# Performance work log

Hardware: AMD Instinct MI355X
Metric: run time of the kernel (lower is better)

The kernel has to match this reference:

```python
import jax, jax.numpy as jnp
import numpy as np

S, D = 8192, 2048      # sequence length, feature dim (input_size)
H, E, K, L = 64, 64, 2, 64  # gate hidden, expert count, top-k, expert layer_size
EPS = 1e-12            # torch F.normalize eps


def setup_inputs() -> dict:
    key = jax.random.key(0)
    ks = jax.random.split(key, 5)
    x = jax.random.normal(ks[0], (S, D), dtype=jnp.float32)
    # torch nn.Linear weights have shape [out_features, in_features]
    Wg_in = jax.random.normal(ks[1], (H, D), dtype=jnp.float32) * 0.02   # gate.input
    Wg_lin = jax.random.normal(ks[2], (E, H), dtype=jnp.float32) * 0.02  # gate.linear
    Wg_out = jax.random.normal(ks[3], (1, S), dtype=jnp.float32) * 0.02  # gate.output
    We = jax.random.normal(ks[4], (E, L, D), dtype=jnp.float32) * 0.02   # expert weight bank
    return {"x": x, "Wg_in": Wg_in, "Wg_lin": Wg_lin, "Wg_out": Wg_out, "We": We}


def reference(x, Wg_in, Wg_lin, Wg_out, We):
    # --- SparseGate (eval mode: dropout = identity) ---
    h = x @ Wg_in.T                         # [S, H]
    logits = h @ Wg_lin.T                   # [S, E]
    scores = (logits.T @ Wg_out.T)[:, 0]    # Linear(S,1) applied to [E,S] -> [E]
    topv, idx = jax.lax.top_k(scores, K)    # global top-k experts for whole input
    g = jax.nn.softmax(topv)                # softmax over the k selected logits

    # --- dispatch to k selected experts (FFNN: Linear -> normalize(-1) -> GELU) ---
    Wsel = We[idx]                          # [K, L, D]
    z = jnp.einsum('sd,kld->ksl', x, Wsel)  # [K, S, L]
    z = z / jnp.maximum(jnp.linalg.norm(z, axis=-1, keepdims=True), EPS)
    z = jax.nn.gelu(z, approximate=False)   # torch GELU default is exact erf

    # --- weighted combine: sum_k g_k * expert_k(x) ---
    return jnp.einsum('k,ksl->sl', g, z)    # [S, L]
```

## Files before the change

kernel.cpp:

```cpp
#include <hip/hip_runtime.h>
#include <hip/hip_bf16.h>
#include <math.h>

#define D_DIM 2048
#define L_DIM 64
#define E_NUM 64
#define H_DIM 64

typedef float f32x4_t __attribute__((ext_vector_type(4)));
typedef unsigned int u32x4_t __attribute__((ext_vector_type(4)));
typedef __bf16 bf16x8_t __attribute__((ext_vector_type(8)));

#define WS_UPART 0u
#define WS_U     (128u * 2048u * 4u)
#define WS_V     (WS_U + 2048u * 4u)
#define WS_META  (WS_V + 256u)
#define WS_WB    (WS_META + 64u)
#define WS_XB    (WS_WB + 128u * 2048u * 2u)

__global__ void k_upart(const float* __restrict__ x, const float* __restrict__ wout,
                        float* __restrict__ upart, __hip_bfloat16* __restrict__ xb) {
  const int d4 = (blockIdx.x * 256 + threadIdx.x) * 4;
  const int s0 = blockIdx.y * 64;
  const float* xp = x + (size_t)s0 * D_DIM + d4;
  float4 acc = make_float4(0.f, 0.f, 0.f, 0.f);
#pragma unroll 4
  for (int i = 0; i < 64; ++i) {
    const float w = wout[s0 + i];
    const f32x4_t xv = __builtin_nontemporal_load(
        reinterpret_cast<const f32x4_t*>(xp + (size_t)i * D_DIM));
    acc.x += xv[0] * w; acc.y += xv[1] * w; acc.z += xv[2] * w; acc.w += xv[3] * w;
    union { __hip_bfloat16 h[4]; uint2 u; } pk;
    pk.h[0] = __float2bfloat16(xv[0]); pk.h[1] = __float2bfloat16(xv[1]);
    pk.h[2] = __float2bfloat16(xv[2]); pk.h[3] = __float2bfloat16(xv[3]);
    *reinterpret_cast<uint2*>(xb + (size_t)(s0 + i) * D_DIM + d4) = pk.u;
  }
  *reinterpret_cast<float4*>(upart + (size_t)blockIdx.y * D_DIM + d4) = acc;
}

__global__ void k_ufinish(const float* __restrict__ upart, float* __restrict__ u) {
  const int d = blockIdx.x * 256 + threadIdx.x;
  float s = 0.f;
#pragma unroll 8
  for (int c = 0; c < 128; ++c) s += upart[(size_t)c * D_DIM + d];
  u[d] = s;
}

__global__ void k_v(const float* __restrict__ wg_in, const float* __restrict__ u,
                    float* __restrict__ v) {
  const int h = blockIdx.x;
  const int t = threadIdx.x;
  const float4* wr = reinterpret_cast<const float4*>(wg_in + (size_t)h * D_DIM);
  const float4* ur = reinterpret_cast<const float4*>(u);
  float s = 0.f;
#pragma unroll
  for (int i = t; i < 512; i += 256) {
    const float4 a = wr[i];
    const float4 b = ur[i];
    s += a.x * b.x + a.y * b.y + a.z * b.z + a.w * b.w;
  }
  __shared__ float red[4];
#pragma unroll
  for (int off = 32; off; off >>= 1) s += __shfl_down(s, off, 64);
  if ((t & 63) == 0) red[t >> 6] = s;
  __syncthreads();
  if (t == 0) v[h] = red[0] + red[1] + red[2] + red[3];
}

__global__ void k_gate(const float* __restrict__ wg_lin, const float* __restrict__ v,
                       int* __restrict__ sel, float* __restrict__ g) {
  __shared__ float vv[H_DIM];
  __shared__ float sc[E_NUM];
  const int t = threadIdx.x;
  vv[t] = v[t];
  __syncthreads();
  float s = 0.f;
#pragma unroll 8
  for (int hh = 0; hh < H_DIM; ++hh) s += wg_lin[t * H_DIM + hh] * vv[hh];
  sc[t] = s;
  __syncthreads();
  if (t == 0) {
    int b1 = 0; float m1 = sc[0];
    for (int e = 1; e < E_NUM; ++e) { if (sc[e] > m1) { m1 = sc[e]; b1 = e; } }
    int b2 = -1; float m2 = -3.4e38f;
    for (int e = 0; e < E_NUM; ++e) {
      if (e != b1 && sc[e] > m2) { m2 = sc[e]; b2 = e; }
    }
    const float e2 = expf(m2 - m1);
    const float g0 = 1.0f / (1.0f + e2);
    sel[0] = b1; sel[1] = b2;
    g[0] = g0; g[1] = 1.0f - g0;
  }
}

__global__ void k_wb(const float* __restrict__ we, const int* __restrict__ sel,
                     __hip_bfloat16* __restrict__ wb) {
  const int n = blockIdx.x;
  const int e = sel[n >> 6];
  const int l = n & 63;
  const float* src = we + ((size_t)e * L_DIM + l) * D_DIM;
  const int t = threadIdx.x;
  const float4 a = reinterpret_cast<const float4*>(src)[2 * t];
  const float4 b = reinterpret_cast<const float4*>(src)[2 * t + 1];
  union { __hip_bfloat16 h[8]; uint4 u; } pk;
  pk.h[0] = __float2bfloat16(a.x); pk.h[1] = __float2bfloat16(a.y);
  pk.h[2] = __float2bfloat16(a.z); pk.h[3] = __float2bfloat16(a.w);
  pk.h[4] = __float2bfloat16(b.x); pk.h[5] = __float2bfloat16(b.y);
  pk.h[6] = __float2bfloat16(b.z); pk.h[7] = __float2bfloat16(b.w);
  reinterpret_cast<uint4*>(wb + (size_t)n * D_DIM)[t] = pk.u;
}

__device__ __forceinline__ void async_ld16(const void* gp, void* lp) {
  __builtin_amdgcn_global_load_lds(
      (const __attribute__((address_space(1))) unsigned int*)gp,
      (__attribute__((address_space(3))) unsigned int*)lp, 16, 0, 0);
}

__device__ __forceinline__ float gelu_f(float v) {
  return 0.5f * v * (1.0f + erff(v * 0.70710678118654752440f));
}

#define STG_BYTES 20480

__global__ __launch_bounds__(1024) void k_moe_gemm(
    const __hip_bfloat16* __restrict__ xb, const __hip_bfloat16* __restrict__ wb,
    const float* __restrict__ gw, float* __restrict__ out) {
  __shared__ __align__(16) unsigned char lds[4 * STG_BYTES];

  const int tid = threadIdx.x;
  const int kg = tid >> 8;
  const int lt = tid & 255;
  const int wc = (tid >> 6) & 3;
  const int lane = tid & 63;
  const int m0 = blockIdx.x * 32;
  const float g0 = gw[0], g1 = gw[1];

  unsigned char* ldsA0 = lds + kg * STG_BYTES;
  unsigned char* ldsB0 = ldsA0 + 32 * 128;

  const int sar = lt >> 3, sap = lt & 7;
  const int sakc = sap ^ (sar & 7);
  const __hip_bfloat16* gA = xb + (size_t)(m0 + sar) * D_DIM + kg * 512 + sakc * 8;
  unsigned char* ldsAw = ldsA0 + lt * 16;

  const int fr = lane & 15, fq = lane >> 4;

  f32x4_t acc00 = {0.f, 0.f, 0.f, 0.f};
  f32x4_t acc01 = acc00, acc10 = acc00, acc11 = acc00;

  for (int kk = 0; kk < 8; ++kk) {
    const int k0 = kg * 512 + kk * 64;
    if (kk) __syncthreads();
    const u32x4_t av = __builtin_nontemporal_load(
        reinterpret_cast<const u32x4_t*>(gA + kk * 64));
#pragma unroll
    for (int i = 0; i < 4; ++i) {
      const int c = i * 256 + lt;
      const int r = c >> 3, p = c & 7;
      const int kc = p ^ (r & 7);
      async_ld16(wb + (size_t)r * D_DIM + k0 + kc * 8, ldsB0 + c * 16);
    }
    *reinterpret_cast<u32x4_t*>(ldsAw) = av;
    __syncthreads();
    union fragu { uint4 u; bf16x8_t v; };
    fragu af[2][2], bfr[2][2];
#pragma unroll
    for (int mt = 0; mt < 2; ++mt)
#pragma unroll
      for (int ks = 0; ks < 2; ++ks) {
        const int ar2 = mt * 16 + fr;
        const int kq = ks * 4 + fq;
        af[mt][ks].u = *reinterpret_cast<const uint4*>(
            ldsA0 + ar2 * 128 + ((kq ^ (ar2 & 7)) * 16));
      }
#pragma unroll
    for (int nt = 0; nt < 2; ++nt)
#pragma unroll
      for (int ks = 0; ks < 2; ++ks) {
        const int r = wc * 32 + nt * 16 + fr;
        const int kq = ks * 4 + fq;
        bfr[nt][ks].u = *reinterpret_cast<const uint4*>(
            ldsB0 + r * 128 + ((kq ^ (r & 7)) * 16));
      }
    acc00 = __builtin_amdgcn_mfma_f32_16x16x32_bf16(af[0][0].v, bfr[0][0].v, acc00, 0, 0, 0);
    acc00 = __builtin_amdgcn_mfma_f32_16x16x32_bf16(af[0][1].v, bfr[0][1].v, acc00, 0, 0, 0);
    acc01 = __builtin_amdgcn_mfma_f32_16x16x32_bf16(af[0][0].v, bfr[1][0].v, acc01, 0, 0, 0);
    acc01 = __builtin_amdgcn_mfma_f32_16x16x32_bf16(af[0][1].v, bfr[1][1].v, acc01, 0, 0, 0);
    acc10 = __builtin_amdgcn_mfma_f32_16x16x32_bf16(af[1][0].v, bfr[0][0].v, acc10, 0, 0, 0);
    acc10 = __builtin_amdgcn_mfma_f32_16x16x32_bf16(af[1][1].v, bfr[0][1].v, acc10, 0, 0, 0);
    acc11 = __builtin_amdgcn_mfma_f32_16x16x32_bf16(af[1][0].v, bfr[1][0].v, acc11, 0, 0, 0);
    acc11 = __builtin_amdgcn_mfma_f32_16x16x32_bf16(af[1][1].v, bfr[1][1].v, acc11, 0, 0, 0);
  }
  __syncthreads();
  {
    float* z = reinterpret_cast<float*>(lds) + kg * (32 * 132);
    const int colbase = wc * 32 + fr;
#pragma unroll
    for (int reg = 0; reg < 4; ++reg) {
      const int r0 = fq * 4 + reg;
      z[r0 * 132 + colbase]             = acc00[reg];
      z[r0 * 132 + colbase + 16]        = acc01[reg];
      z[(16 + r0) * 132 + colbase]      = acc10[reg];
      z[(16 + r0) * 132 + colbase + 16] = acc11[reg];
    }
  }
  __syncthreads();
  {
    float* zb = reinterpret_cast<float*>(lds);
    const int r = tid >> 5;
    const int cb = (tid & 31) * 4;
    const int o = r * 132 + cb;
    f32x4_t s = *reinterpret_cast<f32x4_t*>(zb + o)
              + *reinterpret_cast<f32x4_t*>(zb + 1 * 4224 + o)
              + *reinterpret_cast<f32x4_t*>(zb + 2 * 4224 + o)
              + *reinterpret_cast<f32x4_t*>(zb + 3 * 4224 + o);
    *reinterpret_cast<f32x4_t*>(zb + o) = s;
  }
  __syncthreads();
  float* z = reinterpret_cast<float*>(lds);
  float* ps = reinterpret_cast<float*>(lds + 4 * 16896);
  if (tid < 256) {
    const int r = tid >> 3, seg = tid & 7;
    float s = 0.f;
#pragma unroll
    for (int i2 = 0; i2 < 16; ++i2) {
      const float t2 = z[r * 132 + seg * 16 + i2];
      s += t2 * t2;
    }
    ps[r * 8 + seg] = s;
  }
  __syncthreads();
  if (tid < 256) {
    const int r = tid >> 3, j = tid & 7;
    const float s0 = ps[r * 8 + 0] + ps[r * 8 + 1] + ps[r * 8 + 2] + ps[r * 8 + 3];
    const float s1 = ps[r * 8 + 4] + ps[r * 8 + 5] + ps[r * 8 + 6] + ps[r * 8 + 7];
    const float i0 = 1.0f / fmaxf(sqrtf(s0), 1e-12f);
    const float i1 = 1.0f / fmaxf(sqrtf(s1), 1e-12f);
    float o[8];
#pragma unroll
    for (int i2 = 0; i2 < 8; ++i2) {
      const int c = j * 8 + i2;
      const float za = z[r * 132 + c] * i0;
      const float zb2 = z[r * 132 + 64 + c] * i1;
      o[i2] = g0 * gelu_f(za) + g1 * gelu_f(zb2);
    }
    float4* op = reinterpret_cast<float4*>(out + (size_t)(m0 + r) * 64 + j * 8);
    op[0] = make_float4(o[0], o[1], o[2], o[3]);
    op[1] = make_float4(o[4], o[5], o[6], o[7]);
  }
}

extern "C" void kernel_launch(void* const* d_in, const int* in_sizes, int n_in,
                              void* d_out, int out_size, void* d_ws, size_t ws_size,
                              hipStream_t stream) {
  (void)in_sizes; (void)n_in; (void)out_size; (void)ws_size;
  const float* x      = (const float*)d_in[0];
  const float* wg_in  = (const float*)d_in[1];
  const float* wg_lin = (const float*)d_in[2];
  const float* wg_out = (const float*)d_in[3];
  const float* we     = (const float*)d_in[4];
  float* out = (float*)d_out;
  char* ws = (char*)d_ws;

  float* upart = (float*)(ws + WS_UPART);
  float* u     = (float*)(ws + WS_U);
  float* v     = (float*)(ws + WS_V);
  int*   sel   = (int*)(ws + WS_META);
  float* g     = (float*)(ws + WS_META + 8);
  __hip_bfloat16* wb = (__hip_bfloat16*)(ws + WS_WB);
  __hip_bfloat16* xb = (__hip_bfloat16*)(ws + WS_XB);

  k_upart  <<<dim3(2, 128), 256, 0, stream>>>(x, wg_out, upart, xb);
  k_ufinish<<<8, 256, 0, stream>>>(upart, u);
  k_v      <<<64, 256, 0, stream>>>(wg_in, u, v);
  k_gate   <<<1, 64, 0, stream>>>(wg_lin, v, sel, g);
  k_wb     <<<128, 256, 0, stream>>>(we, sel, wb);
  k_moe_gemm<<<256, 1024, 0, stream>>>(xb, wb, g, out);
}
```

Baseline: 169.1 us.

## Retile MoE GEMM with split-K grid, double-buffered LDS, separate epilogue kernel

The expert GEMM now uses 128-row tiles with a 4-way split-K across the grid. Both operands are staged into double-buffered LDS with async global-to-LDS loads, overlapping the next k-step load with the current MFMAs. Partial sums go to a workspace, and a new finish kernel reduces them and applies normalize, GELU and the gated combine. The x-reduction kernel is also regridded to 512 blocks with 8-wide vectors, and its nontemporal loads are dropped. The cost is extra global traffic for the split-K partials (about 16 MB written and read back) plus one more kernel launch.

```diff
diff --git a/kernel.cpp b/kernel.cpp
--- a/kernel.cpp
+++ b/kernel.cpp
@@ -8,41 +8,46 @@
 #define H_DIM 64
 
 typedef float f32x4_t __attribute__((ext_vector_type(4)));
-typedef unsigned int u32x4_t __attribute__((ext_vector_type(4)));
 typedef __bf16 bf16x8_t __attribute__((ext_vector_type(8)));
 
 #define WS_UPART 0u
-#define WS_U     (128u * 2048u * 4u)
+#define WS_U     (512u * 2048u * 4u)
 #define WS_V     (WS_U + 2048u * 4u)
 #define WS_META  (WS_V + 256u)
 #define WS_WB    (WS_META + 64u)
 #define WS_XB    (WS_WB + 128u * 2048u * 2u)
+#define WS_PART  (WS_XB + 8192u * 2048u * 2u)
 
 __global__ void k_upart(const float* __restrict__ x, const float* __restrict__ wout,
                         float* __restrict__ upart, __hip_bfloat16* __restrict__ xb) {
-  const int d4 = (blockIdx.x * 256 + threadIdx.x) * 4;
-  const int s0 = blockIdx.y * 64;
-  const float* xp = x + (size_t)s0 * D_DIM + d4;
-  float4 acc = make_float4(0.f, 0.f, 0.f, 0.f);
-#pragma unroll 4
-  for (int i = 0; i < 64; ++i) {
+  const int d8 = threadIdx.x * 8;
+  const int s0 = blockIdx.x * 16;
+  float a0 = 0.f, a1 = 0.f, a2 = 0.f, a3 = 0.f;
+  float a4 = 0.f, a5 = 0.f, a6 = 0.f, a7 = 0.f;
+  for (int i = 0; i < 16; ++i) {
+    const size_t row = (size_t)(s0 + i);
     const float w = wout[s0 + i];
-    const f32x4_t xv = __builtin_nontemporal_load(
-        reinterpret_cast<const f32x4_t*>(xp + (size_t)i * D_DIM));
-    acc.x += xv[0] * w; acc.y += xv[1] * w; acc.z += xv[2] * w; acc.w += xv[3] * w;
-    union { __hip_bfloat16 h[4]; uint2 u; } pk;
-    pk.h[0] = __float2bfloat16(xv[0]); pk.h[1] = __float2bfloat16(xv[1]);
-    pk.h[2] = __float2bfloat16(xv[2]); pk.h[3] = __float2bfloat16(xv[3]);
-    *reinterpret_cast<uint2*>(xb + (size_t)(s0 + i) * D_DIM + d4) = pk.u;
-  }
-  *reinterpret_cast<float4*>(upart + (size_t)blockIdx.y * D_DIM + d4) = acc;
+    const float4 pa = *reinterpret_cast<const float4*>(x + row * D_DIM + d8);
+    const float4 pb = *reinterpret_cast<const float4*>(x + row * D_DIM + d8 + 4);
+    a0 += pa.x * w; a1 += pa.y * w; a2 += pa.z * w; a3 += pa.w * w;
+    a4 += pb.x * w; a5 += pb.y * w; a6 += pb.z * w; a7 += pb.w * w;
+    union { __hip_bfloat16 h[8]; uint4 u; } pk;
+    pk.h[0] = __float2bfloat16(pa.x); pk.h[1] = __float2bfloat16(pa.y);
+    pk.h[2] = __float2bfloat16(pa.z); pk.h[3] = __float2bfloat16(pa.w);
+    pk.h[4] = __float2bfloat16(pb.x); pk.h[5] = __float2bfloat16(pb.y);
+    pk.h[6] = __float2bfloat16(pb.z); pk.h[7] = __float2bfloat16(pb.w);
+    *reinterpret_cast<uint4*>(xb + row * D_DIM + d8) = pk.u;
+  }
+  float* up = upart + (size_t)blockIdx.x * D_DIM + d8;
+  *reinterpret_cast<float4*>(up)     = make_float4(a0, a1, a2, a3);
+  *reinterpret_cast<float4*>(up + 4) = make_float4(a4, a5, a6, a7);
 }
 
 __global__ void k_ufinish(const float* __restrict__ upart, float* __restrict__ u) {
   const int d = blockIdx.x * 256 + threadIdx.x;
   float s = 0.f;
 #pragma unroll 8
-  for (int c = 0; c < 128; ++c) s += upart[(size_t)c * D_DIM + d];
+  for (int c = 0; c < 512; ++c) s += upart[(size_t)c * D_DIM + d];
   u[d] = s;
 }
 
@@ -120,106 +125,128 @@
   return 0.5f * v * (1.0f + erff(v * 0.70710678118654752440f));
 }
 
-#define STG_BYTES 20480
-
-__global__ __launch_bounds__(1024) void k_moe_gemm(
+__global__ __launch_bounds__(512) void k_moe_gemm(
     const __hip_bfloat16* __restrict__ xb, const __hip_bfloat16* __restrict__ wb,
-    const float* __restrict__ gw, float* __restrict__ out) {
-  __shared__ __align__(16) unsigned char lds[4 * STG_BYTES];
+    float* __restrict__ part) {
+  __shared__ __align__(16) unsigned char lds[2][32768];
 
   const int tid = threadIdx.x;
-  const int kg = tid >> 8;
-  const int lt = tid & 255;
-  const int wc = (tid >> 6) & 3;
-  const int lane = tid & 63;
+  const int w = tid >> 6, lane = tid & 63;
+  const int wm = w >> 2, wn = w & 3;
+  const int m0 = blockIdx.x * 128;
+  const int kg = blockIdx.y;
+  const int kbase = kg * 512;
+  const int fr = lane & 15, fq = lane >> 4;
+
+  int sr[2], skc[2];
+#pragma unroll
+  for (int ph = 0; ph < 2; ++ph) {
+    const int c = ph * 512 + tid;
+    sr[ph] = c >> 3;
+    skc[ph] = (c & 7) ^ (sr[ph] & 7);
+  }
+
+  f32x4_t acc[4][2];
+#pragma unroll
+  for (int mf = 0; mf < 4; ++mf)
+#pragma unroll
+    for (int nf = 0; nf < 2; ++nf) acc[mf][nf] = (f32x4_t){0.f, 0.f, 0.f, 0.f};
+
+  auto stage = [&](int buf, int kk) {
+    const int koff = kbase + kk * 64;
+#pragma unroll
+    for (int ph = 0; ph < 2; ++ph) {
+      const int c = ph * 512 + tid;
+      async_ld16(xb + (size_t)(m0 + sr[ph]) * D_DIM + koff + skc[ph] * 8,
+                 &lds[buf][c * 16]);
+      async_ld16(wb + (size_t)sr[ph] * D_DIM + koff + skc[ph] * 8,
+                 &lds[buf][16384 + c * 16]);
+    }
+  };
+
+  stage(0, 0);
+  __syncthreads();
+  for (int kk = 0; kk < 8; ++kk) {
+    const int cur = kk & 1;
+    if (kk < 7) stage(cur ^ 1, kk + 1);
+    const unsigned char* ldsA = lds[cur];
+    const unsigned char* ldsB = lds[cur] + 16384;
+    union fragu { uint4 u; bf16x8_t v; };
+    fragu af[4][2], bf_[2][2];
+#pragma unroll
+    for (int mf = 0; mf < 4; ++mf)
+#pragma unroll
+      for (int ks = 0; ks < 2; ++ks) {
+        const int ar = wm * 64 + mf * 16 + fr;
+        const int kq = ks * 4 + fq;
+        af[mf][ks].u = *reinterpret_cast<const uint4*>(
+            ldsA + ar * 128 + ((kq ^ (ar & 7)) * 16));
+      }
+#pragma unroll
+    for (int nf = 0; nf < 2; ++nf)
+#pragma unroll
+      for (int ks = 0; ks < 2; ++ks) {
+        const int br = wn * 32 + nf * 16 + fr;
+        const int kq = ks * 4 + fq;
+        bf_[nf][ks].u = *reinterpret_cast<const uint4*>(
+            ldsB + br * 128 + ((kq ^ (br & 7)) * 16));
+      }
+#pragma unroll
+    for (int mf = 0; mf < 4; ++mf)
+#pragma unroll
+      for (int nf = 0; nf < 2; ++nf) {
+        acc[mf][nf] = __builtin_amdgcn_mfma_f32_16x16x32_bf16(
+            af[mf][0].v, bf_[nf][0].v, acc[mf][nf], 0, 0, 0);
+        acc[mf][nf] = __builtin_amdgcn_mfma_f32_16x16x32_bf16(
+            af[mf][1].v, bf_[nf][1].v, acc[mf][nf], 0, 0, 0);
+      }
+    __syncthreads();
+  }
+
+  float* z = reinterpret_cast<float*>(lds);
+#pragma unroll
+  for (int mf = 0; mf < 4; ++mf)
+#pragma unroll
+    for (int nf = 0; nf < 2; ++nf)
+#pragma unroll
+      for (int reg = 0; reg < 4; ++reg)
+        z[(wm * 64 + mf * 16 + fq * 4 + reg) * 128 + wn * 32 + nf * 16 + fr] =
+            acc[mf][nf][reg];
+  __syncthreads();
+#pragma unroll
+  for (int p = 0; p < 8; ++p) {
+    const int idx = p * 512 + tid;
+    const int r = idx >> 5, c4 = (idx & 31) * 4;
+    *reinterpret_cast<f32x4_t*>(part + ((size_t)kg * 8192 + m0 + r) * 128 + c4) =
+        *reinterpret_cast<const f32x4_t*>(z + r * 128 + c4);
+  }
+}
+
+__global__ __launch_bounds__(256) void k_finish(const float* __restrict__ part,
+                                                const float* __restrict__ gw,
+                                                float* __restrict__ out) {
+  __shared__ float z[32 * 132];
+  __shared__ float ps[32 * 8];
+  const int tid = threadIdx.x;
   const int m0 = blockIdx.x * 32;
   const float g0 = gw[0], g1 = gw[1];
-
-  unsigned char* ldsA0 = lds + kg * STG_BYTES;
-  unsigned char* ldsB0 = ldsA0 + 32 * 128;
-
-  const int sar = lt >> 3, sap = lt & 7;
-  const int sakc = sap ^ (sar & 7);
-  const __hip_bfloat16* gA = xb + (size_t)(m0 + sar) * D_DIM + kg * 512 + sakc * 8;
-  unsigned char* ldsAw = ldsA0 + lt * 16;
-
-  const int fr = lane & 15, fq = lane >> 4;
-
-  f32x4_t acc00 = {0.f, 0.f, 0.f, 0.f};
-  f32x4_t acc01 = acc00, acc10 = acc00, acc11 = acc00;
-
-  for (int kk = 0; kk < 8; ++kk) {
-    const int k0 = kg * 512 + kk * 64;
-    if (kk) __syncthreads();
-    const u32x4_t av = __builtin_nontemporal_load(
-        reinterpret_cast<const u32x4_t*>(gA + kk * 64));
-#pragma unroll
-    for (int i = 0; i < 4; ++i) {
-      const int c = i * 256 + lt;
-      const int r = c >> 3, p = c & 7;
-      const int kc = p ^ (r & 7);
-      async_ld16(wb + (size_t)r * D_DIM + k0 + kc * 8, ldsB0 + c * 16);
-    }
-    *reinterpret_cast<u32x4_t*>(ldsAw) = av;
-    __syncthreads();
-    union fragu { uint4 u; bf16x8_t v; };
-    fragu af[2][2], bfr[2][2];
-#pragma unroll
-    for (int mt = 0; mt < 2; ++mt)
-#pragma unroll
-      for (int ks = 0; ks < 2; ++ks) {
-        const int ar2 = mt * 16 + fr;
-        const int kq = ks * 4 + fq;
-        af[mt][ks].u = *reinterpret_cast<const uint4*>(
-            ldsA0 + ar2 * 128 + ((kq ^ (ar2 & 7)) * 16));
-      }
-#pragma unroll
-    for (int nt = 0; nt < 2; ++nt)
-#pragma unroll
-      for (int ks = 0; ks < 2; ++ks) {
-        const int r = wc * 32 + nt * 16 + fr;
-        const int kq = ks * 4 + fq;
-        bfr[nt][ks].u = *reinterpret_cast<const uint4*>(
-            ldsB0 + r * 128 + ((kq ^ (r & 7)) * 16));
-      }
-    acc00 = __builtin_amdgcn_mfma_f32_16x16x32_bf16(af[0][0].v, bfr[0][0].v, acc00, 0, 0, 0);
-    acc00 = __builtin_amdgcn_mfma_f32_16x16x32_bf16(af[0][1].v, bfr[0][1].v, acc00, 0, 0, 0);
-    acc01 = __builtin_amdgcn_mfma_f32_16x16x32_bf16(af[0][0].v, bfr[1][0].v, acc01, 0, 0, 0);
-    acc01 = __builtin_amdgcn_mfma_f32_16x16x32_bf16(af[0][1].v, bfr[1][1].v, acc01, 0, 0, 0);
-    acc10 = __builtin_amdgcn_mfma_f32_16x16x32_bf16(af[1][0].v, bfr[0][0].v, acc10, 0, 0, 0);
-    acc10 = __builtin_amdgcn_mfma_f32_16x16x32_bf16(af[1][1].v, bfr[0][1].v, acc10, 0, 0, 0);
-    acc11 = __builtin_amdgcn_mfma_f32_16x16x32_bf16(af[1][0].v, bfr[1][0].v, acc11, 0, 0, 0);
-    acc11 = __builtin_amdgcn_mfma_f32_16x16x32_bf16(af[1][1].v, bfr[1][1].v, acc11, 0, 0, 0);
+  const size_t KSTRIDE = (size_t)8192 * 128;
+#pragma unroll
+  for (int p = 0; p < 4; ++p) {
+    const int idx = p * 256 + tid;
+    const int r = idx >> 5, c4 = (idx & 31) * 4;
+    const float* pp = part + ((size_t)(m0 + r)) * 128 + c4;
+    const f32x4_t s = *reinterpret_cast<const f32x4_t*>(pp)
+                    + *reinterpret_cast<const f32x4_t*>(pp + KSTRIDE)
+                    + *reinterpret_cast<const f32x4_t*>(pp + 2 * KSTRIDE)
+                    + *reinterpret_cast<const f32x4_t*>(pp + 3 * KSTRIDE);
+    z[r * 132 + c4 + 0] = s[0];
+    z[r * 132 + c4 + 1] = s[1];
+    z[r * 132 + c4 + 2] = s[2];
+    z[r * 132 + c4 + 3] = s[3];
   }
   __syncthreads();
   {
-    float* z = reinterpret_cast<float*>(lds) + kg * (32 * 132);
-    const int colbase = wc * 32 + fr;
-#pragma unroll
-    for (int reg = 0; reg < 4; ++reg) {
-      const int r0 = fq * 4 + reg;
-      z[r0 * 132 + colbase]             = acc00[reg];
-      z[r0 * 132 + colbase + 16]        = acc01[reg];
-      z[(16 + r0) * 132 + colbase]      = acc10[reg];
-      z[(16 + r0) * 132 + colbase + 16] = acc11[reg];
-    }
-  }
-  __syncthreads();
-  {
-    float* zb = reinterpret_cast<float*>(lds);
-    const int r = tid >> 5;
-    const int cb = (tid & 31) * 4;
-    const int o = r * 132 + cb;
-    f32x4_t s = *reinterpret_cast<f32x4_t*>(zb + o)
-              + *reinterpret_cast<f32x4_t*>(zb + 1 * 4224 + o)
-              + *reinterpret_cast<f32x4_t*>(zb + 2 * 4224 + o)
-              + *reinterpret_cast<f32x4_t*>(zb + 3 * 4224 + o);
-    *reinterpret_cast<f32x4_t*>(zb + o) = s;
-  }
-  __syncthreads();
-  float* z = reinterpret_cast<float*>(lds);
-  float* ps = reinterpret_cast<float*>(lds + 4 * 16896);
-  if (tid < 256) {
     const int r = tid >> 3, seg = tid & 7;
     float s = 0.f;
 #pragma unroll
@@ -230,7 +257,7 @@
     ps[r * 8 + seg] = s;
   }
   __syncthreads();
-  if (tid < 256) {
+  {
     const int r = tid >> 3, j = tid & 7;
     const float s0 = ps[r * 8 + 0] + ps[r * 8 + 1] + ps[r * 8 + 2] + ps[r * 8 + 3];
     const float s1 = ps[r * 8 + 4] + ps[r * 8 + 5] + ps[r * 8 + 6] + ps[r * 8 + 7];
@@ -269,11 +296,13 @@
   float* g     = (float*)(ws + WS_META + 8);
   __hip_bfloat16* wb = (__hip_bfloat16*)(ws + WS_WB);
   __hip_bfloat16* xb = (__hip_bfloat16*)(ws + WS_XB);
-
-  k_upart  <<<dim3(2, 128), 256, 0, stream>>>(x, wg_out, upart, xb);
+  float* part = (float*)(ws + WS_PART);
+
+  k_upart  <<<512, 256, 0, stream>>>(x, wg_out, upart, xb);
   k_ufinish<<<8, 256, 0, stream>>>(upart, u);
   k_v      <<<64, 256, 0, stream>>>(wg_in, u, v);
   k_gate   <<<1, 64, 0, stream>>>(wg_lin, v, sel, g);
   k_wb     <<<128, 256, 0, stream>>>(we, sel, wb);
-  k_moe_gemm<<<256, 1024, 0, stream>>>(xb, wb, g, out);
-}
+  k_moe_gemm<<<dim3(64, 4), 512, 0, stream>>>(xb, wb, part);
+  k_finish <<<256, 256, 0, stream>>>(part, g, out);
+}
```

Measured after the change: 183.1 us. 8.3% more time.
